# Performance work log

Hardware: AMD Instinct MI355X
Metric: run time of the kernel (lower is better)

## Reference

```python
import jax, jax.numpy as jnp
import numpy as np

B, C_IN, IMG, P, G, E, H = 4, 3, 576, 16, 36, 768, 12
T = G * G  # 1296 tokens
HD = E // H  # 64
LN_EPS = 1e-5


def layer_norm(x, g, b):
    mu = jnp.mean(x, axis=-1, keepdims=True)
    var = jnp.mean((x - mu) ** 2, axis=-1, keepdims=True)
    return (x - mu) * jax.lax.rsqrt(var + LN_EPS) * g + b


def setup_inputs() -> dict:
    key = jax.random.key(0)
    ks = jax.random.split(key, 12)
    s = lambda *sh: 0.02
    return {
        "x": jax.random.normal(ks[0], (B, C_IN, IMG, IMG), jnp.float32),
        "conv_w": jax.random.normal(ks[1], (E, C_IN, P, P), jnp.float32) * 0.02,
        "conv_b": jnp.zeros((E,), jnp.float32),
        "wq": jax.random.normal(ks[2], (E, E), jnp.float32) * 0.02,
        "wk": jax.random.normal(ks[3], (E, E), jnp.float32) * 0.02,
        "wv": jax.random.normal(ks[4], (E, E), jnp.float32) * 0.02,
        "wo": jax.random.normal(ks[5], (E, E), jnp.float32) * 0.02,
        "bo": jnp.zeros((E,), jnp.float32),
        "w1": jax.random.normal(ks[6], (E, 4 * E), jnp.float32) * 0.02,
        "b1": jnp.zeros((4 * E,), jnp.float32),
        "w2": jax.random.normal(ks[7], (4 * E, E), jnp.float32) * 0.02,
        "b2": jnp.zeros((E,), jnp.float32),
        "ln1_g": jnp.ones((E,), jnp.float32),
        "ln1_b": jnp.zeros((E,), jnp.float32),
        "ln2_g": jnp.ones((E,), jnp.float32),
        "ln2_b": jnp.zeros((E,), jnp.float32),
    }


def reference(x, conv_w, conv_b, wq, wk, wv, wo, bo, w1, b1, w2, b2,
              ln1_g, ln1_b, ln2_g, ln2_b):
    # --- patch embed: stride==kernel conv as patch reshape + einsum ---
    xr = x.reshape(B, C_IN, G, P, G, P)  # b c i p j q
    tok = jnp.einsum('bcipjq,ecpq->bije', xr, conv_w) + conv_b
    tok = tok.reshape(B, T, E)  # row-major (i,j) matches flatten(2).transpose

    # --- causal multi-head attention (scale uses n_embd, as in source) ---
    h = layer_norm(tok, ln1_g, ln1_b)
    q = (h @ wq).reshape(B, T, H, HD)
    k = (h @ wk).reshape(B, T, H, HD)
    v = (h @ wv).reshape(B, T, H, HD)
    scores = jnp.einsum('bqhd,bkhd->bhqk', q, k) * (E ** -0.5)
    mask = jnp.tril(jnp.ones((T, T), bool))
    scores = jnp.where(mask, scores, -jnp.inf)
    attn = jax.nn.softmax(scores, axis=-1)
    ao = jnp.einsum('bhqk,bkhd->bqhd', attn, v).reshape(B, T, E)
    tok = tok + (ao @ wo + bo)

    # --- MLP ---
    h2 = layer_norm(tok, ln2_g, ln2_b)
    tok = tok + (jax.nn.relu(h2 @ w1 + b1) @ w2 + b2)

    # --- back to image grid ---
    return tok.reshape(B, G, G, E).transpose(0, 3, 1, 2)
```

## Files before the change

kernel.cpp:

```cpp
#include <hip/hip_runtime.h>

typedef unsigned short u16;
typedef unsigned int u32;
typedef unsigned long long u64;
typedef float f32x4 __attribute__((ext_vector_type(4)));
typedef __bf16 bf16x8 __attribute__((ext_vector_type(8)));
typedef __bf16 bf16x4 __attribute__((ext_vector_type(4)));
typedef u16 u16x8 __attribute__((ext_vector_type(8)));

#define DEV __device__ __forceinline__


DEV u16 f2bf(float f) {
    union { float f; u32 u; } un; un.f = f;
    u32 u = un.u;
    return (u16)((u + 0x7fffu + ((u >> 16) & 1u)) >> 16);
}

DEV void gll16(const u16* src, u16* dst) {
    auto g = (const __attribute__((address_space(1))) u32*)(src);
    auto s = (__attribute__((address_space(3))) u32*)(dst);
    __builtin_amdgcn_global_load_lds(g, s, 16, 0, 0);
}

__global__ void convcvt_k(const float* __restrict__ src, u16* __restrict__ dst) {
    int i = blockIdx.x * 256 + threadIdx.x;
    f32x4 v = ((const f32x4*)src)[i];
    union { u16 q[4]; u64 ll; } un;
    #pragma unroll
    for (int j = 0; j < 4; ++j) un.q[j] = f2bf(v[j]);
    ((u64*)dst)[i] = un.ll;
}

__global__ void wtrans_k(const float* __restrict__ src, u16* __restrict__ dst, int K, int N) {
    __shared__ float tile[32][33];
    int n0 = blockIdx.x * 32, k0 = blockIdx.y * 32;
    int tx = threadIdx.x & 31, ty = threadIdx.x >> 5;
    #pragma unroll
    for (int i = 0; i < 32; i += 8)
        tile[ty + i][tx] = src[(size_t)(k0 + ty + i) * N + n0 + tx];
    __syncthreads();
    #pragma unroll
    for (int i = 0; i < 32; i += 8)
        dst[(size_t)(n0 + ty + i) * K + k0 + tx] = f2bf(tile[tx][ty + i]);
}

__global__ void patch_k(const float* __restrict__ x, u16* __restrict__ out) {
    int idx = blockIdx.x * 256 + threadIdx.x;
    int j = idx % 36; int r1 = idx / 36;
    int p = r1 % 16;  int r2 = r1 / 16;
    int i = r2 % 36;  int r3 = r2 / 36;
    int c = r3 % 3;   int b = r3 / 3;
    const f32x4* src = (const f32x4*)(x + (size_t)((b * 3 + c) * 576 + i * 16 + p) * 576 + j * 16);
    u16x8 lo, hi;
    #pragma unroll
    for (int k = 0; k < 2; ++k) {
        f32x4 v = src[k];
        #pragma unroll
        for (int e = 0; e < 4; ++e) lo[k * 4 + e] = f2bf(v[e]);
    }
    #pragma unroll
    for (int k = 0; k < 2; ++k) {
        f32x4 v = src[2 + k];
        #pragma unroll
        for (int e = 0; e < 4; ++e) hi[k * 4 + e] = f2bf(v[e]);
    }
    u16* dst = out + (size_t)(b * 1296 + i * 36 + j) * 768 + c * 256 + p * 16;
    *(u16x8*)dst = lo;
    *(u16x8*)(dst + 8) = hi;
}

__global__ __launch_bounds__(256) void ln_k(const float* __restrict__ x, const float* __restrict__ g,
                                            const float* __restrict__ bta, u16* __restrict__ out) {
    int row = blockIdx.x * 4 + (threadIdx.x >> 6);
    int l = threadIdx.x & 63;
    const float* xr = x + (size_t)row * 768;
    float v[12]; float s = 0.f, s2 = 0.f;
    #pragma unroll
    for (int i = 0; i < 12; ++i) { v[i] = xr[l + 64 * i]; s += v[i]; s2 += v[i] * v[i]; }
    #pragma unroll
    for (int off = 32; off; off >>= 1) { s += __shfl_xor(s, off); s2 += __shfl_xor(s2, off); }
    float mu = s * (1.f / 768.f);
    float var = s2 * (1.f / 768.f) - mu * mu;
    float rs = rsqrtf(var + 1e-5f);
    u16* orow = out + (size_t)row * 768;
    #pragma unroll
    for (int i = 0; i < 12; ++i) {
        int c = l + 64 * i;
        orow[c] = f2bf((v[i] - mu) * rs * g[c] + bta[c]);
    }
}

__global__ void vtrans_k(const u16* __restrict__ qkv, u16* __restrict__ vt) {
    __shared__ u16 tile[32][33];
    int bh = blockIdx.z; int b = bh / 12, h = bh % 12;
    int t0 = blockIdx.x * 32, d0 = blockIdx.y * 32;
    int tx = threadIdx.x & 31, ty = threadIdx.x >> 5;
    #pragma unroll
    for (int i = 0; i < 32; i += 8) {
        int t = t0 + ty + i; int tc = min(t, 1295);
        tile[ty + i][tx] = qkv[(size_t)(b * 1296 + tc) * 2304 + 1536 + h * 64 + d0 + tx];
    }
    __syncthreads();
    #pragma unroll
    for (int i = 0; i < 32; i += 8) {
        int d = d0 + ty + i; int t = t0 + tx;
        if (t < 1296) vt[(size_t)(bh * 64 + d) * 1344 + t] = tile[tx][ty + i];
    }
}

template <int BN, int EPI>
__global__ __launch_bounds__(256) void gemm_k(const u16* __restrict__ A, const u16* __restrict__ Bt,
                                              const float* __restrict__ bias, const float* __restrict__ resid,
                                              void* __restrict__ Cout, int K, int ldc, int nbx) {
    constexpr int M = 5184;
    constexpr int NF = BN / 32;
    __shared__ __align__(16) u16 lds[2][(128 + BN) * 64];
    const int tid = threadIdx.x;
    const int l = tid & 63, w = tid >> 6;
    const int lr = l & 15, lq = l >> 4;
    const int wm = w >> 1, wn = w & 1;

    const int total = nbx * 41;
    const int q = total >> 3, r = total & 7;
    const int x = blockIdx.x & 7;
    const int j = blockIdx.x >> 3;
    const int wrk = x * q + min(x, r) + j;
    const int by = wrk / nbx, bx = wrk - by * nbx;
    const int bm = by * 128;
    const int bn = bx * BN;

    f32x4 acc[4][NF];
    f32x4 zz = {0.f, 0.f, 0.f, 0.f};
    #pragma unroll
    for (int i = 0; i < 4; ++i)
        #pragma unroll
        for (int jj = 0; jj < NF; ++jj) acc[i][jj] = zz;

    const int nk = K >> 6;

    auto stage = [&](int buf, int kt) {
        u16* abase = &lds[buf][0];
        #pragma unroll
        for (int i = 0; i < 4; ++i) {
            int slot = tid + i * 256;
            int row = slot >> 3, piece = slot & 7;
            int sp = piece ^ (row & 7);
            const u16* src = A + (size_t)min(bm + row, M - 1) * K + kt * 64 + sp * 8;
            gll16(src, abase + ((tid & ~63) + i * 256) * 8);
        }
        u16* bbase = &lds[buf][128 * 64];
        #pragma unroll
        for (int i = 0; i < NF; ++i) {
            int slot = tid + i * 256;
            int row = slot >> 3, piece = slot & 7;
            int sp = piece ^ (row & 7);
            const u16* src = Bt + (size_t)(bn + row) * K + kt * 64 + sp * 8;
            gll16(src, bbase + ((tid & ~63) + i * 256) * 8);
        }
    };

    stage(0, 0);
    for (int kt = 0; kt < nk; ++kt) {
        const int cur = kt & 1;
        if (kt + 1 < nk) {
            stage(cur ^ 1, kt + 1);
            if constexpr (BN == 128) asm volatile("s_waitcnt vmcnt(8)\ns_barrier" ::: "memory");
            else                     asm volatile("s_waitcnt vmcnt(6)\ns_barrier" ::: "memory");
        } else {
            asm volatile("s_waitcnt vmcnt(0)\ns_barrier" ::: "memory");
        }
        bf16x8 af[4][2], bfr[NF][2];
        #pragma unroll
        for (int mi = 0; mi < 4; ++mi) {
            int row = wm * 64 + mi * 16 + lr;
            #pragma unroll
            for (int ks = 0; ks < 2; ++ks)
                af[mi][ks] = *(const bf16x8*)&lds[cur][row * 64 + (((lq + 4 * ks) ^ (row & 7)) << 3)];
        }
        #pragma unroll
        for (int ni = 0; ni < NF; ++ni) {
            int row = wn * (BN / 2) + ni * 16 + lr;
            #pragma unroll
            for (int ks = 0; ks < 2; ++ks)
                bfr[ni][ks] = *(const bf16x8*)&lds[cur][128 * 64 + row * 64 + (((lq + 4 * ks) ^ (row & 7)) << 3)];
        }
        #pragma unroll
        for (int mi = 0; mi < 4; ++mi)
            #pragma unroll
            for (int ni = 0; ni < NF; ++ni) {
                acc[mi][ni] = __builtin_amdgcn_mfma_f32_16x16x32_bf16(af[mi][0], bfr[ni][0], acc[mi][ni], 0, 0, 0);
                acc[mi][ni] = __builtin_amdgcn_mfma_f32_16x16x32_bf16(af[mi][1], bfr[ni][1], acc[mi][ni], 0, 0, 0);
            }
        asm volatile("s_barrier" ::: "memory");
    }

    #pragma unroll
    for (int mi = 0; mi < 4; ++mi) {
        #pragma unroll
        for (int ni = 0; ni < NF; ++ni) {
            int col = bn + wn * (BN / 2) + ni * 16 + lr;
            float bv = 0.f;
            if constexpr (EPI != 1) bv = bias[col];
            #pragma unroll
            for (int rr = 0; rr < 4; ++rr) {
                int m = bm + wm * 64 + mi * 16 + 4 * lq + rr;
                if (m < M) {
                    float v = acc[mi][ni][rr] + bv;
                    if constexpr (EPI == 2) v = fmaxf(v, 0.f);
                    if constexpr (EPI == 3 || EPI == 4) v += resid[(size_t)m * ldc + col];
                    if constexpr (EPI == 0 || EPI == 3) {
                        ((float*)Cout)[(size_t)m * ldc + col] = v;
                    } else if constexpr (EPI == 4) {
                        int b = m / 1296, t = m - b * 1296;
                        ((float*)Cout)[(size_t)(b * 768 + col) * 1296 + t] = v;
                    } else {
                        ((u16*)Cout)[(size_t)m * ldc + col] = f2bf(v);
                    }
                }
            }
        }
    }
}

__global__ __launch_bounds__(256, 2) void attn_k(const u16* __restrict__ qkv, const u16* __restrict__ vt,
                                                 u16* __restrict__ ao) {
    const float SCALE = 0.03608439182435161f;
    __shared__ __align__(16) u16 kv[2][2][4096];
    __shared__ __align__(16) u16 plds[4][16 * 72];
    const int tid = threadIdx.x;
    const int wid = tid >> 6, l = tid & 63;
    const int id = blockIdx.x;
    const int xr = id & 7, sl = id >> 3;
    const int g = sl / 11, bx = sl - g * 11;
    const int bh = g * 8 + xr;
    const int b = bh / 12, h = bh % 12;
    const int uu = bx * 4 + wid;
    const int u = min(uu, 40);
    const bool valid = (uu <= 40);
    const int lr = l & 15, lq = l >> 4;
    const int q0S = 16 * u, q0L = 16 * (80 - u);
    const bool hasS = valid && (u < 40);
    const int nktS = (u < 40) ? (((q0S + 15) >> 6) + 1) : 0;
    const int nktL = ((q0L + 15) >> 6) + 1;
    const int umin = min(bx * 4, 40);
    const int nktmax = ((16 * (80 - umin) + 15) >> 6) + 1;

    const u16* kbase = qkv + (size_t)(b * 1296) * 2304 + 768 + h * 64;
    const u16* vbase = vt + (size_t)bh * 64 * 1344;
    u16* pl = &plds[wid][0];

    const u16* qpS = qkv + (size_t)(b * 1296 + q0S + lr) * 2304 + h * 64;
    const u16* qpL = qkv + (size_t)(b * 1296 + q0L + lr) * 2304 + h * 64;
    bf16x8 qS0 = *(const bf16x8*)(qpS + 8 * lq);
    bf16x8 qS1 = *(const bf16x8*)(qpS + 32 + 8 * lq);
    bf16x8 qL0 = *(const bf16x8*)(qpL + 8 * lq);
    bf16x8 qL1 = *(const bf16x8*)(qpL + 32 + 8 * lq);

    f32x4 zz = {0.f, 0.f, 0.f, 0.f};
    const float NEG = -__builtin_inff();
    f32x4 oS[4], oL[4];
    float mS = NEG, mL = NEG, lS = 0.f, lL = 0.f;
    #pragma unroll
    for (int i = 0; i < 4; ++i) { oS[i] = zz; oL[i] = zz; }

    auto stage = [&](int buf, int kt) {
        const int k0 = kt * 64;
        #pragma unroll
        for (int i = 0; i < 2; ++i) {
            int slot = tid + i * 256;
            int row = slot >> 3;
            int piece = slot & 7;
            int sp = piece ^ (row & 7);
            int tc = min(k0 + row, 1295);
            gll16(kbase + (size_t)tc * 2304 + sp * 8,
                  &kv[buf][0][((tid & 0xFFFFFFC0) + i * 256) * 8]);
        }
        #pragma unroll
        for (int i = 0; i < 2; ++i) {
            int slot = tid + i * 256;
            int row = slot >> 3;
            int piece = slot & 7;
            int sp = piece ^ (row & 7);
            gll16(vbase + (size_t)row * 1344 + k0 + sp * 8,
                  &kv[buf][1][((tid & 0xFFFFFFC0) + i * 256) * 8]);
        }
    };

    bf16x8 kb[4][2], vb[4][2];

    auto visit = [&](int q0, bf16x8 qa0, bf16x8 qa1, f32x4 (&o)[4],
                     float& mrow, float& lsum, int k0) {
        const int qrow = q0 + lr;
        f32x4 s[4];
        __builtin_amdgcn_s_setprio(1);
        #pragma unroll
        for (int nt = 0; nt < 4; ++nt) {
            f32x4 a = zz;
            a = __builtin_amdgcn_mfma_f32_16x16x32_bf16(kb[nt][0], qa0, a, 0, 0, 0);
            a = __builtin_amdgcn_mfma_f32_16x16x32_bf16(kb[nt][1], qa1, a, 0, 0, 0);
            s[nt] = a;
        }
        __builtin_amdgcn_s_setprio(0);
        float mnt[4];
        #pragma unroll
        for (int nt = 0; nt < 4; ++nt) {
            #pragma unroll
            for (int r = 0; r < 4; ++r) {
                int k = k0 + nt * 16 + 4 * lq + r;
                s[nt][r] = (k <= qrow) ? s[nt][r] : NEG;
            }
            mnt[nt] = fmaxf(fmaxf(s[nt][0], s[nt][1]), fmaxf(s[nt][2], s[nt][3]));
        }
        float mx = fmaxf(fmaxf(mnt[0], mnt[1]), fmaxf(mnt[2], mnt[3]));
        mx = fmaxf(mx, __shfl_xor(mx, 16));
        mx = fmaxf(mx, __shfl_xor(mx, 32));
        float nm = fmaxf(mrow, mx);
        float alpha = __expf(SCALE * (mrow - nm));
        mrow = nm;
        float nbase = -SCALE * nm;
        float tnt[4];
        #pragma unroll
        for (int nt = 0; nt < 4; ++nt) {
            #pragma unroll
            for (int r = 0; r < 4; ++r) {
                float p = __expf(fmaf(s[nt][r], SCALE, nbase));
                s[nt][r] = p;
            }
            tnt[nt] = (s[nt][0] + s[nt][1]) + (s[nt][2] + s[nt][3]);
        }
        float ts = (tnt[0] + tnt[1]) + (tnt[2] + tnt[3]);
        ts += __shfl_xor(ts, 16);
        ts += __shfl_xor(ts, 32);
        lsum = lsum * alpha + ts;
        #pragma unroll
        for (int dt = 0; dt < 4; ++dt) o[dt] *= alpha;
        #pragma unroll
        for (int nt = 0; nt < 4; ++nt) {
            bf16x4 pv = __builtin_convertvector(s[nt], bf16x4);
            *(bf16x4*)&pl[lr * 72 + nt * 16 + 4 * lq] = pv;
        }
        __builtin_amdgcn_wave_barrier();
        bf16x8 pa0 = *(const bf16x8*)&pl[lr * 72 + 8 * lq];
        bf16x8 pa1 = *(const bf16x8*)&pl[lr * 72 + 32 + 8 * lq];
        __builtin_amdgcn_s_setprio(1);
        #pragma unroll
        for (int dt = 0; dt < 4; ++dt) {
            o[dt] = __builtin_amdgcn_mfma_f32_16x16x32_bf16(vb[dt][0], pa0, o[dt], 0, 0, 0);
            o[dt] = __builtin_amdgcn_mfma_f32_16x16x32_bf16(vb[dt][1], pa1, o[dt], 0, 0, 0);
        }
        __builtin_amdgcn_s_setprio(0);
        __builtin_amdgcn_wave_barrier();
    };

    stage(0, 0);
    for (int kt = 0; kt < nktmax; ++kt) {
        const int cur = kt & 1;
        const int k0 = kt * 64;
        __syncthreads();
        if (kt + 1 < nktmax) stage(cur ^ 1, kt + 1);
        #pragma unroll
        for (int nt = 0; nt < 4; ++nt) {
            int krow = nt * 16 + lr;
            kb[nt][0] = *(const bf16x8*)&kv[cur][0][krow * 64 + ((lq ^ (krow & 7)) << 3)];
            kb[nt][1] = *(const bf16x8*)&kv[cur][0][krow * 64 + (((lq + 4) ^ (krow & 7)) << 3)];
        }
        #pragma unroll
        for (int dt = 0; dt < 4; ++dt) {
            int vrow = dt * 16 + lr;
            vb[dt][0] = *(const bf16x8*)&kv[cur][1][vrow * 64 + ((lq ^ (vrow & 7)) << 3)];
            vb[dt][1] = *(const bf16x8*)&kv[cur][1][vrow * 64 + (((lq + 4) ^ (vrow & 7)) << 3)];
        }
        if (valid && kt < nktS) visit(q0S, qS0, qS1, oS, mS, lS, k0);
        if (valid && kt < nktL) visit(q0L, qL0, qL1, oL, mL, lL, k0);
    }

    if (valid) {
        if (hasS) {
            float inv = 1.f / lS;
            u16* aoS = ao + (size_t)(b * 1296 + q0S + lr) * 768 + h * 64 + 4 * lq;
            #pragma unroll
            for (int dt = 0; dt < 4; ++dt) {
                f32x4 ov = oS[dt] * inv;
                *(bf16x4*)(aoS + dt * 16) = __builtin_convertvector(ov, bf16x4);
            }
        }
        float invL = 1.f / lL;
        u16* aoL = ao + (size_t)(b * 1296 + q0L + lr) * 768 + h * 64 + 4 * lq;
        #pragma unroll
        for (int dt = 0; dt < 4; ++dt) {
            f32x4 ov = oL[dt] * invL;
            *(bf16x4*)(aoL + dt * 16) = __builtin_convertvector(ov, bf16x4);
        }
    }
}

extern "C" void kernel_launch(void* const* d_in, const int* in_sizes, int n_in,
                              void* d_out, int out_size, void* d_ws, size_t ws_size,
                              hipStream_t stream) {
    const float* x      = (const float*)d_in[0];
    const float* conv_w = (const float*)d_in[1];
    const float* conv_b = (const float*)d_in[2];
    const float* wq     = (const float*)d_in[3];
    const float* wk     = (const float*)d_in[4];
    const float* wv     = (const float*)d_in[5];
    const float* wo     = (const float*)d_in[6];
    const float* bo     = (const float*)d_in[7];
    const float* w1     = (const float*)d_in[8];
    const float* b1     = (const float*)d_in[9];
    const float* w2     = (const float*)d_in[10];
    const float* b2     = (const float*)d_in[11];
    const float* ln1g   = (const float*)d_in[12];
    const float* ln1b   = (const float*)d_in[13];
    const float* ln2g   = (const float*)d_in[14];
    const float* ln2b   = (const float*)d_in[15];

    char* ws = (char*)d_ws;
    size_t off = 0;
    auto alloc = [&](size_t bytes) { char* p = ws + off; off = (off + bytes + 255) & ~(size_t)255; return p; };
    u16*   convw_bf = (u16*)alloc((size_t)768 * 768 * 2);
    u16*   wqkv_t   = (u16*)alloc((size_t)2304 * 768 * 2);
    u16*   wo_t     = (u16*)alloc((size_t)768 * 768 * 2);
    u16*   w1_t     = (u16*)alloc((size_t)3072 * 768 * 2);
    u16*   w2_t     = (u16*)alloc((size_t)768 * 3072 * 2);
    float* tok      = (float*)alloc((size_t)5184 * 768 * 4);
    u16*   hbuf     = (u16*)alloc((size_t)5184 * 768 * 2);
    u16*   apao     = (u16*)alloc((size_t)5184 * 768 * 2);
    size_t qkv_bytes = ((size_t)5184 * 2304 * 2 + 255) & ~(size_t)255;
    size_t vt_bytes  = (size_t)48 * 64 * 1344 * 2;
    size_t a1_bytes  = (size_t)5184 * 3072 * 2;
    size_t big_bytes = qkv_bytes + vt_bytes;
    if (a1_bytes > big_bytes) big_bytes = a1_bytes;
    char* big = alloc(big_bytes);
    u16* qkvb = (u16*)big;
    u16* vtb  = (u16*)(big + qkv_bytes);
    u16* a1   = (u16*)big;

    convcvt_k<<<576, 256, 0, stream>>>(conv_w, convw_bf);
    wtrans_k<<<dim3(24, 24), 256, 0, stream>>>(wq, wqkv_t, 768, 768);
    wtrans_k<<<dim3(24, 24), 256, 0, stream>>>(wk, wqkv_t + 768 * 768, 768, 768);
    wtrans_k<<<dim3(24, 24), 256, 0, stream>>>(wv, wqkv_t + 2 * 768 * 768, 768, 768);
    wtrans_k<<<dim3(24, 24), 256, 0, stream>>>(wo, wo_t, 768, 768);
    wtrans_k<<<dim3(96, 24), 256, 0, stream>>>(w1, w1_t, 768, 3072);
    wtrans_k<<<dim3(24, 96), 256, 0, stream>>>(w2, w2_t, 3072, 768);
    patch_k<<<972, 256, 0, stream>>>(x, apao);
    gemm_k<64, 0><<<12 * 41, 256, 0, stream>>>(apao, convw_bf, conv_b, nullptr, tok, 768, 768, 12);
    ln_k<<<1296, 256, 0, stream>>>(tok, ln1g, ln1b, hbuf);
    gemm_k<128, 1><<<18 * 41, 256, 0, stream>>>(hbuf, wqkv_t, nullptr, nullptr, qkvb, 768, 2304, 18);
    vtrans_k<<<dim3(41, 2, 48), 256, 0, stream>>>(qkvb, vtb);
    attn_k<<<528, 256, 0, stream>>>(qkvb, vtb, apao);
    gemm_k<64, 3><<<12 * 41, 256, 0, stream>>>(apao, wo_t, bo, tok, tok, 768, 768, 12);
    ln_k<<<1296, 256, 0, stream>>>(tok, ln2g, ln2b, hbuf);
    gemm_k<128, 2><<<24 * 41, 256, 0, stream>>>(hbuf, w1_t, b1, nullptr, a1, 768, 3072, 24);
    gemm_k<64, 4><<<12 * 41, 256, 0, stream>>>(a1, w2_t, b2, tok, d_out, 3072, 768, 12);
}
```

Before: 330.9 us.

## Merge prep kernels, fuse V transpose into QKV GEMM, interleave attention tiles

All weight conversion and transpose kernels plus the patch extraction are merged into a single prep launch, cutting eight launches to one. The QKV GEMM epilogue now writes V directly in transposed layout, so the separate vtrans kernel is gone. The attention inner loop processes the short and long query tiles together when both are active, interleaving their MFMA and softmax work for more ILP. This uses a larger per-wave P buffer and more registers, which may reduce occupancy, and the transposed V stores are strided 8-byte writes.

```diff
diff --git a/kernel.cpp b/kernel.cpp
--- a/kernel.cpp
+++ b/kernel.cpp
@@ -23,18 +23,62 @@
     __builtin_amdgcn_global_load_lds(g, s, 16, 0, 0);
 }
 
-__global__ void convcvt_k(const float* __restrict__ src, u16* __restrict__ dst) {
-    int i = blockIdx.x * 256 + threadIdx.x;
-    f32x4 v = ((const f32x4*)src)[i];
-    union { u16 q[4]; u64 ll; } un;
-    #pragma unroll
-    for (int j = 0; j < 4; ++j) un.q[j] = f2bf(v[j]);
-    ((u64*)dst)[i] = un.ll;
-}
-
-__global__ void wtrans_k(const float* __restrict__ src, u16* __restrict__ dst, int K, int N) {
+__global__ __launch_bounds__(256) void prep_k(
+    const float* __restrict__ x, const float* __restrict__ conv_w,
+    const float* __restrict__ wq, const float* __restrict__ wk,
+    const float* __restrict__ wv, const float* __restrict__ wo,
+    const float* __restrict__ w1, const float* __restrict__ w2,
+    u16* __restrict__ patches, u16* __restrict__ convw_bf,
+    u16* __restrict__ wqkv_t, u16* __restrict__ wo_t,
+    u16* __restrict__ w1_t, u16* __restrict__ w2_t) {
     __shared__ float tile[32][33];
-    int n0 = blockIdx.x * 32, k0 = blockIdx.y * 32;
+    int id = blockIdx.x;
+    if (id < 972) {
+        int idx = id * 256 + threadIdx.x;
+        int j = idx % 36; int r1 = idx / 36;
+        int p = r1 % 16;  int r2 = r1 / 16;
+        int i = r2 % 36;  int r3 = r2 / 36;
+        int c = r3 % 3;   int b = r3 / 3;
+        const f32x4* src = (const f32x4*)(x + (size_t)((b * 3 + c) * 576 + i * 16 + p) * 576 + j * 16);
+        u16x8 lo, hi;
+        #pragma unroll
+        for (int k = 0; k < 2; ++k) {
+            f32x4 v = src[k];
+            #pragma unroll
+            for (int e = 0; e < 4; ++e) lo[k * 4 + e] = f2bf(v[e]);
+        }
+        #pragma unroll
+        for (int k = 0; k < 2; ++k) {
+            f32x4 v = src[2 + k];
+            #pragma unroll
+            for (int e = 0; e < 4; ++e) hi[k * 4 + e] = f2bf(v[e]);
+        }
+        u16* dst = patches + (size_t)(b * 1296 + i * 36 + j) * 768 + c * 256 + p * 16;
+        *(u16x8*)dst = lo;
+        *(u16x8*)(dst + 8) = hi;
+        return;
+    }
+    id -= 972;
+    if (id < 576) {
+        int i = id * 256 + threadIdx.x;
+        f32x4 v = ((const f32x4*)conv_w)[i];
+        union { u16 q[4]; u64 ll; } un;
+        #pragma unroll
+        for (int jj = 0; jj < 4; ++jj) un.q[jj] = f2bf(v[jj]);
+        ((u64*)convw_bf)[i] = un.ll;
+        return;
+    }
+    id -= 576;
+    const float* src; u16* dst; int K, N;
+    if (id < 576)       { src = wq; dst = wqkv_t;                 K = 768;  N = 768; }
+    else if (id < 1152) { src = wk; dst = wqkv_t + 768 * 768;     K = 768;  N = 768;  id -= 576; }
+    else if (id < 1728) { src = wv; dst = wqkv_t + 2 * 768 * 768; K = 768;  N = 768;  id -= 1152; }
+    else if (id < 2304) { src = wo; dst = wo_t;                   K = 768;  N = 768;  id -= 1728; }
+    else if (id < 4608) { src = w1; dst = w1_t;                   K = 768;  N = 3072; id -= 2304; }
+    else                { src = w2; dst = w2_t;                   K = 3072; N = 768;  id -= 4608; }
+    int nbx = N >> 5;
+    int bx = id % nbx, by = id / nbx;
+    int n0 = bx * 32, k0 = by * 32;
     int tx = threadIdx.x & 31, ty = threadIdx.x >> 5;
     #pragma unroll
     for (int i = 0; i < 32; i += 8)
@@ -43,31 +87,6 @@
     #pragma unroll
     for (int i = 0; i < 32; i += 8)
         dst[(size_t)(n0 + ty + i) * K + k0 + tx] = f2bf(tile[tx][ty + i]);
-}
-
-__global__ void patch_k(const float* __restrict__ x, u16* __restrict__ out) {
-    int idx = blockIdx.x * 256 + threadIdx.x;
-    int j = idx % 36; int r1 = idx / 36;
-    int p = r1 % 16;  int r2 = r1 / 16;
-    int i = r2 % 36;  int r3 = r2 / 36;
-    int c = r3 % 3;   int b = r3 / 3;
-    const f32x4* src = (const f32x4*)(x + (size_t)((b * 3 + c) * 576 + i * 16 + p) * 576 + j * 16);
-    u16x8 lo, hi;
-    #pragma unroll
-    for (int k = 0; k < 2; ++k) {
-        f32x4 v = src[k];
-        #pragma unroll
-        for (int e = 0; e < 4; ++e) lo[k * 4 + e] = f2bf(v[e]);
-    }
-    #pragma unroll
-    for (int k = 0; k < 2; ++k) {
-        f32x4 v = src[2 + k];
-        #pragma unroll
-        for (int e = 0; e < 4; ++e) hi[k * 4 + e] = f2bf(v[e]);
-    }
-    u16* dst = out + (size_t)(b * 1296 + i * 36 + j) * 768 + c * 256 + p * 16;
-    *(u16x8*)dst = lo;
-    *(u16x8*)(dst + 8) = hi;
 }
 
 __global__ __launch_bounds__(256) void ln_k(const float* __restrict__ x, const float* __restrict__ g,
@@ -91,27 +110,10 @@
     }
 }
 
-__global__ void vtrans_k(const u16* __restrict__ qkv, u16* __restrict__ vt) {
-    __shared__ u16 tile[32][33];
-    int bh = blockIdx.z; int b = bh / 12, h = bh % 12;
-    int t0 = blockIdx.x * 32, d0 = blockIdx.y * 32;
-    int tx = threadIdx.x & 31, ty = threadIdx.x >> 5;
-    #pragma unroll
-    for (int i = 0; i < 32; i += 8) {
-        int t = t0 + ty + i; int tc = min(t, 1295);
-        tile[ty + i][tx] = qkv[(size_t)(b * 1296 + tc) * 2304 + 1536 + h * 64 + d0 + tx];
-    }
-    __syncthreads();
-    #pragma unroll
-    for (int i = 0; i < 32; i += 8) {
-        int d = d0 + ty + i; int t = t0 + tx;
-        if (t < 1296) vt[(size_t)(bh * 64 + d) * 1344 + t] = tile[tx][ty + i];
-    }
-}
-
 template <int BN, int EPI>
 __global__ __launch_bounds__(256) void gemm_k(const u16* __restrict__ A, const u16* __restrict__ Bt,
                                               const float* __restrict__ bias, const float* __restrict__ resid,
+                                              u16* __restrict__ vtout,
                                               void* __restrict__ Cout, int K, int ldc, int nbx) {
     constexpr int M = 5184;
     constexpr int NF = BN / 32;
@@ -202,20 +204,37 @@
             int col = bn + wn * (BN / 2) + ni * 16 + lr;
             float bv = 0.f;
             if constexpr (EPI != 1) bv = bias[col];
-            #pragma unroll
-            for (int rr = 0; rr < 4; ++rr) {
-                int m = bm + wm * 64 + mi * 16 + 4 * lq + rr;
-                if (m < M) {
-                    float v = acc[mi][ni][rr] + bv;
-                    if constexpr (EPI == 2) v = fmaxf(v, 0.f);
-                    if constexpr (EPI == 3 || EPI == 4) v += resid[(size_t)m * ldc + col];
-                    if constexpr (EPI == 0 || EPI == 3) {
-                        ((float*)Cout)[(size_t)m * ldc + col] = v;
-                    } else if constexpr (EPI == 4) {
-                        int b = m / 1296, t = m - b * 1296;
-                        ((float*)Cout)[(size_t)(b * 768 + col) * 1296 + t] = v;
+            if constexpr (EPI == 1) {
+                int m0 = bm + wm * 64 + mi * 16 + 4 * lq;
+                if (m0 < M) {
+                    if (col < 1536) {
+                        #pragma unroll
+                        for (int rr = 0; rr < 4; ++rr)
+                            ((u16*)Cout)[(size_t)(m0 + rr) * ldc + col] = f2bf(acc[mi][ni][rr]);
                     } else {
-                        ((u16*)Cout)[(size_t)m * ldc + col] = f2bf(v);
+                        int bb = m0 / 1296, t = m0 - bb * 1296;
+                        int d = col - 1536;
+                        int bh = bb * 12 + (d >> 6), dd = d & 63;
+                        bf16x4 pv = __builtin_convertvector(acc[mi][ni], bf16x4);
+                        *(bf16x4*)&vtout[(size_t)(bh * 64 + dd) * 1344 + t] = pv;
+                    }
+                }
+            } else {
+                #pragma unroll
+                for (int rr = 0; rr < 4; ++rr) {
+                    int m = bm + wm * 64 + mi * 16 + 4 * lq + rr;
+                    if (m < M) {
+                        float v = acc[mi][ni][rr] + bv;
+                        if constexpr (EPI == 2) v = fmaxf(v, 0.f);
+                        if constexpr (EPI == 3 || EPI == 4) v += resid[(size_t)m * ldc + col];
+                        if constexpr (EPI == 0 || EPI == 3) {
+                            ((float*)Cout)[(size_t)m * ldc + col] = v;
+                        } else if constexpr (EPI == 4) {
+                            int b = m / 1296, t = m - b * 1296;
+                            ((float*)Cout)[(size_t)(b * 768 + col) * 1296 + t] = v;
+                        } else {
+                            ((u16*)Cout)[(size_t)m * ldc + col] = f2bf(v);
+                        }
                     }
                 }
             }
@@ -227,7 +246,7 @@
                                                  u16* __restrict__ ao) {
     const float SCALE = 0.03608439182435161f;
     __shared__ __align__(16) u16 kv[2][2][4096];
-    __shared__ __align__(16) u16 plds[4][16 * 72];
+    __shared__ __align__(16) u16 plds[4][2 * 16 * 72];
     const int tid = threadIdx.x;
     const int wid = tid >> 6, l = tid & 63;
     const int id = blockIdx.x;
@@ -248,7 +267,8 @@
 
     const u16* kbase = qkv + (size_t)(b * 1296) * 2304 + 768 + h * 64;
     const u16* vbase = vt + (size_t)bh * 64 * 1344;
-    u16* pl = &plds[wid][0];
+    u16* plS = &plds[wid][0];
+    u16* plL = &plds[wid][16 * 72];
 
     const u16* qpS = qkv + (size_t)(b * 1296 + q0S + lr) * 2304 + h * 64;
     const u16* qpL = qkv + (size_t)(b * 1296 + q0L + lr) * 2304 + h * 64;
@@ -269,8 +289,7 @@
         #pragma unroll
         for (int i = 0; i < 2; ++i) {
             int slot = tid + i * 256;
-            int row = slot >> 3;
-            int piece = slot & 7;
+            int row = slot >> 3, piece = slot & 7;
             int sp = piece ^ (row & 7);
             int tc = min(k0 + row, 1295);
             gll16(kbase + (size_t)tc * 2304 + sp * 8,
@@ -279,8 +298,7 @@
         #pragma unroll
         for (int i = 0; i < 2; ++i) {
             int slot = tid + i * 256;
-            int row = slot >> 3;
-            int piece = slot & 7;
+            int row = slot >> 3, piece = slot & 7;
             int sp = piece ^ (row & 7);
             gll16(vbase + (size_t)row * 1344 + k0 + sp * 8,
                   &kv[buf][1][((tid & 0xFFFFFFC0) + i * 256) * 8]);
@@ -288,70 +306,6 @@
     };
 
     bf16x8 kb[4][2], vb[4][2];
-
-    auto visit = [&](int q0, bf16x8 qa0, bf16x8 qa1, f32x4 (&o)[4],
-                     float& mrow, float& lsum, int k0) {
-        const int qrow = q0 + lr;
-        f32x4 s[4];
-        __builtin_amdgcn_s_setprio(1);
-        #pragma unroll
-        for (int nt = 0; nt < 4; ++nt) {
-            f32x4 a = zz;
-            a = __builtin_amdgcn_mfma_f32_16x16x32_bf16(kb[nt][0], qa0, a, 0, 0, 0);
-            a = __builtin_amdgcn_mfma_f32_16x16x32_bf16(kb[nt][1], qa1, a, 0, 0, 0);
-            s[nt] = a;
-        }
-        __builtin_amdgcn_s_setprio(0);
-        float mnt[4];
-        #pragma unroll
-        for (int nt = 0; nt < 4; ++nt) {
-            #pragma unroll
-            for (int r = 0; r < 4; ++r) {
-                int k = k0 + nt * 16 + 4 * lq + r;
-                s[nt][r] = (k <= qrow) ? s[nt][r] : NEG;
-            }
-            mnt[nt] = fmaxf(fmaxf(s[nt][0], s[nt][1]), fmaxf(s[nt][2], s[nt][3]));
-        }
-        float mx = fmaxf(fmaxf(mnt[0], mnt[1]), fmaxf(mnt[2], mnt[3]));
-        mx = fmaxf(mx, __shfl_xor(mx, 16));
-        mx = fmaxf(mx, __shfl_xor(mx, 32));
-        float nm = fmaxf(mrow, mx);
-        float alpha = __expf(SCALE * (mrow - nm));
-        mrow = nm;
-        float nbase = -SCALE * nm;
-        float tnt[4];
-        #pragma unroll
-        for (int nt = 0; nt < 4; ++nt) {
-            #pragma unroll
-            for (int r = 0; r < 4; ++r) {
-                float p = __expf(fmaf(s[nt][r], SCALE, nbase));
-                s[nt][r] = p;
-            }
-            tnt[nt] = (s[nt][0] + s[nt][1]) + (s[nt][2] + s[nt][3]);
-        }
-        float ts = (tnt[0] + tnt[1]) + (tnt[2] + tnt[3]);
-        ts += __shfl_xor(ts, 16);
-        ts += __shfl_xor(ts, 32);
-        lsum = lsum * alpha + ts;
-        #pragma unroll
-        for (int dt = 0; dt < 4; ++dt) o[dt] *= alpha;
-        #pragma unroll
-        for (int nt = 0; nt < 4; ++nt) {
-            bf16x4 pv = __builtin_convertvector(s[nt], bf16x4);
-            *(bf16x4*)&pl[lr * 72 + nt * 16 + 4 * lq] = pv;
-        }
-        __builtin_amdgcn_wave_barrier();
-        bf16x8 pa0 = *(const bf16x8*)&pl[lr * 72 + 8 * lq];
-        bf16x8 pa1 = *(const bf16x8*)&pl[lr * 72 + 32 + 8 * lq];
-        __builtin_amdgcn_s_setprio(1);
-        #pragma unroll
-        for (int dt = 0; dt < 4; ++dt) {
-            o[dt] = __builtin_amdgcn_mfma_f32_16x16x32_bf16(vb[dt][0], pa0, o[dt], 0, 0, 0);
-            o[dt] = __builtin_amdgcn_mfma_f32_16x16x32_bf16(vb[dt][1], pa1, o[dt], 0, 0, 0);
-        }
-        __builtin_amdgcn_s_setprio(0);
-        __builtin_amdgcn_wave_barrier();
-    };
 
     stage(0, 0);
     for (int kt = 0; kt < nktmax; ++kt) {
@@ -371,8 +325,143 @@
             vb[dt][0] = *(const bf16x8*)&kv[cur][1][vrow * 64 + ((lq ^ (vrow & 7)) << 3)];
             vb[dt][1] = *(const bf16x8*)&kv[cur][1][vrow * 64 + (((lq + 4) ^ (vrow & 7)) << 3)];
         }
-        if (valid && kt < nktS) visit(q0S, qS0, qS1, oS, mS, lS, k0);
-        if (valid && kt < nktL) visit(q0L, qL0, qL1, oL, mL, lL, k0);
+        const bool doS = valid && (kt < nktS);
+        const bool doL = valid && (kt < nktL);
+        if (doS) {
+            const int qrS = q0S + lr, qrL = q0L + lr;
+            f32x4 sS[4], sL[4];
+            __builtin_amdgcn_s_setprio(1);
+            #pragma unroll
+            for (int nt = 0; nt < 4; ++nt) {
+                f32x4 a = zz;
+                a = __builtin_amdgcn_mfma_f32_16x16x32_bf16(kb[nt][0], qS0, a, 0, 0, 0);
+                a = __builtin_amdgcn_mfma_f32_16x16x32_bf16(kb[nt][1], qS1, a, 0, 0, 0);
+                sS[nt] = a;
+            }
+            #pragma unroll
+            for (int nt = 0; nt < 4; ++nt) {
+                f32x4 a = zz;
+                a = __builtin_amdgcn_mfma_f32_16x16x32_bf16(kb[nt][0], qL0, a, 0, 0, 0);
+                a = __builtin_amdgcn_mfma_f32_16x16x32_bf16(kb[nt][1], qL1, a, 0, 0, 0);
+                sL[nt] = a;
+            }
+            __builtin_amdgcn_s_setprio(0);
+            float mntS[4], mntL[4];
+            #pragma unroll
+            for (int nt = 0; nt < 4; ++nt) {
+                #pragma unroll
+                for (int r = 0; r < 4; ++r) {
+                    int k = k0 + nt * 16 + 4 * lq + r;
+                    sS[nt][r] = (k <= qrS) ? sS[nt][r] : NEG;
+                    sL[nt][r] = (k <= qrL) ? sL[nt][r] : NEG;
+                }
+                mntS[nt] = fmaxf(fmaxf(sS[nt][0], sS[nt][1]), fmaxf(sS[nt][2], sS[nt][3]));
+                mntL[nt] = fmaxf(fmaxf(sL[nt][0], sL[nt][1]), fmaxf(sL[nt][2], sL[nt][3]));
+            }
+            float mxS = fmaxf(fmaxf(mntS[0], mntS[1]), fmaxf(mntS[2], mntS[3]));
+            float mxL = fmaxf(fmaxf(mntL[0], mntL[1]), fmaxf(mntL[2], mntL[3]));
+            mxS = fmaxf(mxS, __shfl_xor(mxS, 16));
+            mxL = fmaxf(mxL, __shfl_xor(mxL, 16));
+            mxS = fmaxf(mxS, __shfl_xor(mxS, 32));
+            mxL = fmaxf(mxL, __shfl_xor(mxL, 32));
+            float nmS = fmaxf(mS, mxS), nmL = fmaxf(mL, mxL);
+            float aS = __expf(SCALE * (mS - nmS)), aL = __expf(SCALE * (mL - nmL));
+            mS = nmS; mL = nmL;
+            float nbS = -SCALE * nmS, nbL = -SCALE * nmL;
+            float tS = 0.f, tL = 0.f;
+            #pragma unroll
+            for (int nt = 0; nt < 4; ++nt) {
+                #pragma unroll
+                for (int r = 0; r < 4; ++r) {
+                    sS[nt][r] = __expf(fmaf(sS[nt][r], SCALE, nbS));
+                    sL[nt][r] = __expf(fmaf(sL[nt][r], SCALE, nbL));
+                }
+                tS += (sS[nt][0] + sS[nt][1]) + (sS[nt][2] + sS[nt][3]);
+                tL += (sL[nt][0] + sL[nt][1]) + (sL[nt][2] + sL[nt][3]);
+            }
+            tS += __shfl_xor(tS, 16); tL += __shfl_xor(tL, 16);
+            tS += __shfl_xor(tS, 32); tL += __shfl_xor(tL, 32);
+            lS = lS * aS + tS;
+            lL = lL * aL + tL;
+            #pragma unroll
+            for (int dt = 0; dt < 4; ++dt) { oS[dt] *= aS; oL[dt] *= aL; }
+            #pragma unroll
+            for (int nt = 0; nt < 4; ++nt) {
+                *(bf16x4*)&plS[lr * 72 + nt * 16 + 4 * lq] = __builtin_convertvector(sS[nt], bf16x4);
+                *(bf16x4*)&plL[lr * 72 + nt * 16 + 4 * lq] = __builtin_convertvector(sL[nt], bf16x4);
+            }
+            __builtin_amdgcn_wave_barrier();
+            bf16x8 paS0 = *(const bf16x8*)&plS[lr * 72 + 8 * lq];
+            bf16x8 paS1 = *(const bf16x8*)&plS[lr * 72 + 32 + 8 * lq];
+            bf16x8 paL0 = *(const bf16x8*)&plL[lr * 72 + 8 * lq];
+            bf16x8 paL1 = *(const bf16x8*)&plL[lr * 72 + 32 + 8 * lq];
+            __builtin_amdgcn_s_setprio(1);
+            #pragma unroll
+            for (int dt = 0; dt < 4; ++dt) {
+                oS[dt] = __builtin_amdgcn_mfma_f32_16x16x32_bf16(vb[dt][0], paS0, oS[dt], 0, 0, 0);
+                oS[dt] = __builtin_amdgcn_mfma_f32_16x16x32_bf16(vb[dt][1], paS1, oS[dt], 0, 0, 0);
+                oL[dt] = __builtin_amdgcn_mfma_f32_16x16x32_bf16(vb[dt][0], paL0, oL[dt], 0, 0, 0);
+                oL[dt] = __builtin_amdgcn_mfma_f32_16x16x32_bf16(vb[dt][1], paL1, oL[dt], 0, 0, 0);
+            }
+            __builtin_amdgcn_s_setprio(0);
+            __builtin_amdgcn_wave_barrier();
+        } else if (doL) {
+            const int qrL = q0L + lr;
+            f32x4 sL[4];
+            __builtin_amdgcn_s_setprio(1);
+            #pragma unroll
+            for (int nt = 0; nt < 4; ++nt) {
+                f32x4 a = zz;
+                a = __builtin_amdgcn_mfma_f32_16x16x32_bf16(kb[nt][0], qL0, a, 0, 0, 0);
+                a = __builtin_amdgcn_mfma_f32_16x16x32_bf16(kb[nt][1], qL1, a, 0, 0, 0);
+                sL[nt] = a;
+            }
+            __builtin_amdgcn_s_setprio(0);
+            float mntL[4];
+            #pragma unroll
+            for (int nt = 0; nt < 4; ++nt) {
+                #pragma unroll
+                for (int r = 0; r < 4; ++r) {
+                    int k = k0 + nt * 16 + 4 * lq + r;
+                    sL[nt][r] = (k <= qrL) ? sL[nt][r] : NEG;
+                }
+                mntL[nt] = fmaxf(fmaxf(sL[nt][0], sL[nt][1]), fmaxf(sL[nt][2], sL[nt][3]));
+            }
+            float mxL = fmaxf(fmaxf(mntL[0], mntL[1]), fmaxf(mntL[2], mntL[3]));
+            mxL = fmaxf(mxL, __shfl_xor(mxL, 16));
+            mxL = fmaxf(mxL, __shfl_xor(mxL, 32));
+            float nmL = fmaxf(mL, mxL);
+            float aL = __expf(SCALE * (mL - nmL));
+            mL = nmL;
+            float nbL = -SCALE * nmL;
+            float tL = 0.f;
+            #pragma unroll
+            for (int nt = 0; nt < 4; ++nt) {
+                #pragma unroll
+                for (int r = 0; r < 4; ++r)
+                    sL[nt][r] = __expf(fmaf(sL[nt][r], SCALE, nbL));
+                tL += (sL[nt][0] + sL[nt][1]) + (sL[nt][2] + sL[nt][3]);
+            }
+            tL += __shfl_xor(tL, 16);
+            tL += __shfl_xor(tL, 32);
+            lL = lL * aL + tL;
+            #pragma unroll
+            for (int dt = 0; dt < 4; ++dt) oL[dt] *= aL;
+            #pragma unroll
+            for (int nt = 0; nt < 4; ++nt)
+                *(bf16x4*)&plL[lr * 72 + nt * 16 + 4 * lq] = __builtin_convertvector(sL[nt], bf16x4);
+            __builtin_amdgcn_wave_barrier();
+            bf16x8 paL0 = *(const bf16x8*)&plL[lr * 72 + 8 * lq];
+            bf16x8 paL1 = *(const bf16x8*)&plL[lr * 72 + 32 + 8 * lq];
+            __builtin_amdgcn_s_setprio(1);
+            #pragma unroll
+            for (int dt = 0; dt < 4; ++dt) {
+                oL[dt] = __builtin_amdgcn_mfma_f32_16x16x32_bf16(vb[dt][0], paL0, oL[dt], 0, 0, 0);
+                oL[dt] = __builtin_amdgcn_mfma_f32_16x16x32_bf16(vb[dt][1], paL1, oL[dt], 0, 0, 0);
+            }
+            __builtin_amdgcn_s_setprio(0);
+            __builtin_amdgcn_wave_barrier();
+        }
     }
 
     if (valid) {
@@ -436,21 +525,14 @@
     u16* vtb  = (u16*)(big + qkv_bytes);
     u16* a1   = (u16*)big;
 
-    convcvt_k<<<576, 256, 0, stream>>>(conv_w, convw_bf);
-    wtrans_k<<<dim3(24, 24), 256, 0, stream>>>(wq, wqkv_t, 768, 768);
-    wtrans_k<<<dim3(24, 24), 256, 0, stream>>>(wk, wqkv_t + 768 * 768, 768, 768);
-    wtrans_k<<<dim3(24, 24), 256, 0, stream>>>(wv, wqkv_t + 2 * 768 * 768, 768, 768);
-    wtrans_k<<<dim3(24, 24), 256, 0, stream>>>(wo, wo_t, 768, 768);
-    wtrans_k<<<dim3(96, 24), 256, 0, stream>>>(w1, w1_t, 768, 3072);
-    wtrans_k<<<dim3(24, 96), 256, 0, stream>>>(w2, w2_t, 3072, 768);
-    patch_k<<<972, 256, 0, stream>>>(x, apao);
-    gemm_k<64, 0><<<12 * 41, 256, 0, stream>>>(apao, convw_bf, conv_b, nullptr, tok, 768, 768, 12);
+    prep_k<<<8460, 256, 0, stream>>>(x, conv_w, wq, wk, wv, wo, w1, w2,
+                                     apao, convw_bf, wqkv_t, wo_t, w1_t, w2_t);
+    gemm_k<64, 0><<<12 * 41, 256, 0, stream>>>(apao, convw_bf, conv_b, nullptr, nullptr, tok, 768, 768, 12);
     ln_k<<<1296, 256, 0, stream>>>(tok, ln1g, ln1b, hbuf);
-    gemm_k<128, 1><<<18 * 41, 256, 0, stream>>>(hbuf, wqkv_t, nullptr, nullptr, qkvb, 768, 2304, 18);
-    vtrans_k<<<dim3(41, 2, 48), 256, 0, stream>>>(qkvb, vtb);
+    gemm_k<128, 1><<<18 * 41, 256, 0, stream>>>(hbuf, wqkv_t, nullptr, nullptr, vtb, qkvb, 768, 2304, 18);
     attn_k<<<528, 256, 0, stream>>>(qkvb, vtb, apao);
-    gemm_k<64, 3><<<12 * 41, 256, 0, stream>>>(apao, wo_t, bo, tok, tok, 768, 768, 12);
+    gemm_k<64, 3><<<12 * 41, 256, 0, stream>>>(apao, wo_t, bo, tok, nullptr, tok, 768, 768, 12);
     ln_k<<<1296, 256, 0, stream>>>(tok, ln2g, ln2b, hbuf);
-    gemm_k<128, 2><<<24 * 41, 256, 0, stream>>>(hbuf, w1_t, b1, nullptr, a1, 768, 3072, 24);
-    gemm_k<64, 4><<<12 * 41, 256, 0, stream>>>(a1, w2_t, b2, tok, d_out, 3072, 768, 12);
-}
+    gemm_k<128, 2><<<24 * 41, 256, 0, stream>>>(hbuf, w1_t, b1, nullptr, nullptr, a1, 768, 3072, 24);
+    gemm_k<64, 4><<<12 * 41, 256, 0, stream>>>(a1, w2_t, b2, tok, nullptr, d_out, 3072, 768, 12);
+}
```

Measured after the change: 313.3 us. -5.3%, faster.
